# Performance work log

Measured on AMD Instinct MI355X. Metric: run time of the kernel, lower is better.

The kernel has to match this reference:

```python
import jax, jax.numpy as jnp
import numpy as np

NB, FD, NR, L = 4, 128, 4, 4
CUT, CUT3, NE = 5.0, 4.0, 108
N_ATOMS, N_EDGES, N_ANGLES, N_GRAPHS = 8000, 200000, 400000, 100
BONDS_PER, ANGLES_PER = 2000, 4000

def swish(x):
    return x * jax.nn.sigmoid(x)

def cutoff_fn(r, rc):
    x = r / rc
    return 1.0 - 6.0 * x**5 + 15.0 * x**4 - 10.0 * x**3

def rbf(r):
    # smooth Bessel basis, [E, NR+1]
    n = jnp.arange(1, NR + 2, dtype=r.dtype)
    return jnp.sqrt(2.0 / CUT) * jnp.sin(n * jnp.pi * r[:, None] / CUT) / r[:, None]

def shrb(r, cos_t):
    # spherical-harmonic (Legendre, l=0..3) x radial Bessel (n=1..4) -> [A, 16]
    n = jnp.arange(1, NR + 1, dtype=r.dtype)
    rad = jnp.sin(n * jnp.pi * r[:, None] / CUT3) / r[:, None]
    ang = jnp.stack([jnp.ones_like(cos_t), cos_t, 0.5 * (3.0 * cos_t**2 - 1.0), 0.5 * (5.0 * cos_t**3 - 3.0 * cos_t)], axis=1)
    feat = (rad[:, :, None] * ang[:, None, :]).reshape(r.shape[0], NR * L)
    return feat * cutoff_fn(r, CUT3)[:, None]

def setup_inputs() -> dict:
    key = jax.random.key(0)
    ks = jax.random.split(key, 24)
    def nrm(k, shape, fan):
        return jax.random.normal(k, shape, jnp.float32) / np.sqrt(fan).astype(np.float32)
    return {
        'atomic_numbers': jax.random.randint(ks[0], (N_ATOMS,), 0, NE, jnp.int32),
        'edge_index': jax.random.randint(ks[1], (2, N_EDGES), 0, N_ATOMS, jnp.int32),
        'edge_dist': jax.random.uniform(ks[2], (N_EDGES,), jnp.float32, 0.5, CUT),
        'three_body_indices': jax.random.randint(ks[3], (N_ANGLES, 2), 0, BONDS_PER, jnp.int32),
        'norm_ik': jax.random.uniform(ks[4], (N_ANGLES,), jnp.float32, 0.5, CUT3),
        'cos_angles': jax.random.uniform(ks[5], (N_ANGLES,), jnp.float32, -1.0, 1.0),
        'total_num_bonds': jnp.full((N_GRAPHS,), BONDS_PER, jnp.int32),
        'total_num_angles': jnp.full((N_GRAPHS,), ANGLES_PER, jnp.int32),
        'emb': nrm(ks[6], (NE, FD), 1.0),
        'W_enc': nrm(ks[7], (NR + 1, FD), NR + 1), 'b_enc': jnp.zeros((FD,), jnp.float32),
        'W_angle': nrm(ks[8], (NB, NR * L, FD), NR * L),
        'Wg': nrm(ks[9], (NB, FD, FD), FD), 'bg': jnp.zeros((NB, FD), jnp.float32),
        'W_tb': nrm(ks[10], (NB, FD, FD), FD), 'b_tb': jnp.zeros((NB, FD), jnp.float32),
        'We1': nrm(ks[11], (NB, 3 * FD, FD), 3 * FD), 'be1': jnp.zeros((NB, FD), jnp.float32),
        'We0': nrm(ks[12], (NB, NR + 1, FD), NR + 1),
        'Wa1': nrm(ks[13], (NB, 3 * FD, FD), 3 * FD), 'ba1': jnp.zeros((NB, FD), jnp.float32),
        'Wa0': nrm(ks[14], (NB, NR + 1, FD), NR + 1),
        'W1': nrm(ks[15], (FD, FD), FD), 'b1': jnp.zeros((FD,), jnp.float32),
        'W2': nrm(ks[16], (FD, FD), FD), 'b2': jnp.zeros((FD,), jnp.float32),
        'W3': nrm(ks[17], (FD, 1), FD), 'b3': jnp.zeros((1,), jnp.float32),
    }

def reference(atomic_numbers, edge_index, edge_dist, three_body_indices, norm_ik, cos_angles, total_num_bonds, total_num_angles, emb, W_enc, b_enc, W_angle, Wg, bg, W_tb, b_tb, We1, be1, We0, Wa1, ba1, Wa0, W1, b1, W2, b2, W3, b3):
    E, N, A = edge_dist.shape[0], atomic_numbers.shape[0], norm_ik.shape[0]
    # ragged three-body index offsets (cumsum over per-graph bond counts)
    cum = jnp.cumsum(total_num_bonds)
    off = jnp.concatenate([jnp.zeros((1,), cum.dtype), cum[:-1]])
    off_a = jnp.repeat(off, total_num_angles, total_repeat_length=A)
    tbi = three_body_indices + off_a[:, None].astype(three_body_indices.dtype)
    idx_ij, idx_ik = tbi[:, 0], tbi[:, 1]
    send, recv = edge_index[0], edge_index[1]
    ef0 = rbf(edge_dist)                      # [E, 5]
    e = swish(ef0 @ W_enc + b_enc)            # [E, FD]
    v = emb[atomic_numbers]                   # [N, FD]
    ang = shrb(norm_ik, cos_angles)           # [A, 16]
    fc_ik = cutoff_fn(norm_ik, CUT3)          # [A]
    for b in range(NB):
        # three-body interaction: angle -> center bond ij
        k_atom = recv[idx_ik]
        gate = jax.nn.sigmoid(v[k_atom] @ Wg[b] + bg[b])            # [A, FD]
        msg = (ang @ W_angle[b]) * gate * fc_ik[:, None]            # [A, FD]
        agg = jax.ops.segment_sum(msg, idx_ij, num_segments=E)      # [E, FD]
        e = e + swish(agg @ W_tb[b] + b_tb[b])
        # gated graph conv: edge update then atom update
        vi, vj = v[send], v[recv]
        h = jnp.concatenate([vi, vj, e], axis=1)                    # [E, 3FD]
        e = e + swish(h @ We1[b] + be1[b]) * (ef0 @ We0[b])
        h2 = jnp.concatenate([vi, vj, e], axis=1)
        m = swish(h2 @ Wa1[b] + ba1[b]) * (ef0 @ Wa0[b])
        v = v + jax.ops.segment_sum(m, recv, num_segments=N)
    # per-atom energy readout
    h = swish(v @ W1 + b1)
    h = swish(h @ W2 + b2)
    return h @ W3 + b3                                              # [N, 1]
```

## Files before the change

kernel.cpp:

```cpp
#include <hip/hip_runtime.h>


typedef short short8 __attribute__((ext_vector_type(8)));
typedef float f32x4v __attribute__((ext_vector_type(4)));
typedef __bf16 bf16x2_t __attribute__((ext_vector_type(2)));

__device__ __forceinline__ float sigmoidf_(float x) { return 1.0f / (1.0f + __expf(-x)); }
__device__ __forceinline__ float swishf_(float x) { return x * sigmoidf_(x); }

__device__ __forceinline__ unsigned int pk2(float a, float b) {
    bf16x2_t v = {(__bf16)a, (__bf16)b};
    return __builtin_bit_cast(unsigned int, v);
}
__device__ __forceinline__ unsigned short f2bf(float x) {
    return __builtin_bit_cast(unsigned short, (__bf16)x);
}
__device__ __forceinline__ float bf2f(unsigned short u) {
    return __uint_as_float(((unsigned int)u) << 16);
}
__device__ __forceinline__ float blo(unsigned int u) { return __uint_as_float(u << 16); }
__device__ __forceinline__ float bhi(unsigned int u) { return __uint_as_float(u & 0xffff0000u); }
__device__ __forceinline__ unsigned int addbf2(unsigned int a, unsigned int b) {
    return pk2(blo(a) + blo(b), bhi(a) + bhi(b));
}

__device__ __forceinline__ f32x4v mfma_bf16(short8 a, short8 b, f32x4v c) {
    return __builtin_amdgcn_mfma_f32_16x16x32_bf16(a, b, c, 0, 0, 0);
}

__device__ __forceinline__ float4 f4add(float4 a, float4 b) {
    return make_float4(a.x + b.x, a.y + b.y, a.z + b.z, a.w + b.w);
}
__device__ __forceinline__ float4 f4swish(float4 a) {
    return make_float4(swishf_(a.x), swishf_(a.y), swishf_(a.z), swishf_(a.w));
}
__device__ __forceinline__ float getc(const float4& v, int i) {
    return i == 0 ? v.x : (i == 1 ? v.y : (i == 2 ? v.z : v.w));
}

#define FMA4(J, A) \
    acc[J].x = fmaf(A, bv.x, acc[J].x); acc[J].y = fmaf(A, bv.y, acc[J].y); \
    acc[J].z = fmaf(A, bv.z, acc[J].z); acc[J].w = fmaf(A, bv.w, acc[J].w)

template <int S>
__device__ __forceinline__ void gemm32f(const float* As, const float* __restrict__ B,
                                        int tm, int f0, float4 acc[4]) {
#pragma unroll 4
    for (int k = 0; k < 128; ++k) {
        const float4 a0 = *(const float4*)(As + k * S + (tm << 2));
        const float4 bv = *(const float4*)(B + (k << 7) + f0);
        FMA4(0, a0.x); FMA4(1, a0.y); FMA4(2, a0.z); FMA4(3, a0.w);
    }
}

__global__ void k_offsets(const int* __restrict__ tnb, const int* __restrict__ tna,
                          int NG, int* __restrict__ boff, int* __restrict__ acum) {
    if (threadIdx.x == 0 && blockIdx.x == 0) {
        int ab = 0, aa = 0;
        for (int g = 0; g < NG; ++g) {
            boff[g] = ab;
            ab += tnb[g];
            aa += tna[g];
            acum[g] = aa;
        }
    }
}

__global__ void k_hist_ang(const int* __restrict__ tb,
                           const int* __restrict__ boff, const int* __restrict__ acum,
                           int A, int NG, int* __restrict__ cnt) {
    const int a = blockIdx.x * 256 + threadIdx.x;
    if (a >= A) return;
    int lo = 0, hi = NG - 1;
    while (lo < hi) {
        const int mid = (lo + hi) >> 1;
        if (a < acum[mid]) hi = mid; else lo = mid + 1;
    }
    atomicAdd(&cnt[tb[2 * a] + boff[lo]], 1);
}

__global__ void k_angle_scatter(const int* __restrict__ tb, const float* __restrict__ rnorm,
                                const float* __restrict__ cosang, const int* __restrict__ ei,
                                int E, int A, int NG,
                                const int* __restrict__ boff, const int* __restrict__ acum,
                                const int* __restrict__ start, const int* __restrict__ bsumE,
                                int* __restrict__ fill,
                                unsigned short* __restrict__ angS,
                                int* __restrict__ katS) {
    const int a = blockIdx.x * 256 + threadIdx.x;
    if (a >= A) return;
    int lo = 0, hi = NG - 1;
    while (lo < hi) {
        const int mid = (lo + hi) >> 1;
        if (a < acum[mid]) hi = mid; else lo = mid + 1;
    }
    const int off = boff[lo];
    const int ij = tb[2 * a] + off;
    const int kat = ei[(size_t)E + tb[2 * a + 1] + off];
    const int pos = start[ij] + bsumE[ij >> 11] + atomicAdd(&fill[ij], 1);

    const float r = rnorm[a], c = cosang[a];
    const float rinv = 1.0f / r;
    const float x = r * 0.25f;
    const float fc = 1.0f + x * x * x * (-10.0f + x * (15.0f - 6.0f * x));
    const float fc2 = fc * fc;
    const float p2 = 1.5f * c * c - 0.5f;
    const float p3 = 2.5f * c * c * c - 1.5f * c;
    union { unsigned int ui[8]; uint4 v[2]; } pkk;
#pragma unroll
    for (int n = 0; n < 4; ++n) {
        const float rad = __sinf(r * (float)(n + 1) * 0.7853981633974483f) * rinv * fc2;
        pkk.ui[n * 2 + 0] = pk2(rad, rad * c);
        pkk.ui[n * 2 + 1] = pk2(rad * p2, rad * p3);
    }
    uint4* dst = (uint4*)(angS + (size_t)pos * 16);
    dst[0] = pkk.v[0];
    dst[1] = pkk.v[1];
    katS[pos] = kat;
}

__global__ void k_scan1b(const int* __restrict__ cntE, int* __restrict__ startE,
                         int* __restrict__ bsumE, int nE, int nbE,
                         int* __restrict__ fillE,
                         const int* __restrict__ cntRi, int* __restrict__ startRi,
                         int* __restrict__ bsumRi, int nR,
                         int* __restrict__ fillRi) {
    __shared__ int sh[256];
    const int b = blockIdx.x;
    const int* cnt; int* start; int* bsum; int* fill; int n; int blk;
    if (b < nbE) { cnt = cntE;  start = startE;  bsum = bsumE;  fill = fillE;  n = nE; blk = b; }
    else         { cnt = cntRi; start = startRi; bsum = bsumRi; fill = fillRi; n = nR; blk = b - nbE; }
    const int t = threadIdx.x;
    const int base = blk * 2048 + t * 8;
    int v[8], s = 0;
#pragma unroll
    for (int i = 0; i < 8; ++i) { v[i] = (base + i < n) ? cnt[base + i] : 0; s += v[i]; }
    sh[t] = s;
    __syncthreads();
    for (int off = 1; off < 256; off <<= 1) {
        int x = (t >= off) ? sh[t - off] : 0;
        __syncthreads();
        sh[t] += x;
        __syncthreads();
    }
    if (t == 255) bsum[blk] = sh[255];
    int run = sh[t] - s;
#pragma unroll
    for (int i = 0; i < 8; ++i) {
        if (base + i < n) { start[base + i] = run; fill[base + i] = 0; }
        run += v[i];
    }
}

__global__ void k_scan2b(int* __restrict__ bsumE, int nbE,
                         int* __restrict__ bsumRi, int nbR) {
    __shared__ int sh[256];
    int* bsum; int nb;
    if (blockIdx.x == 0) { bsum = bsumE; nb = nbE; }
    else                 { bsum = bsumRi; nb = nbR; }
    const int t = threadIdx.x;
    int v = (t < nb) ? bsum[t] : 0;
    sh[t] = v;
    __syncthreads();
    for (int off = 1; off < 256; off <<= 1) {
        int x = (t >= off) ? sh[t - off] : 0;
        __syncthreads();
        sh[t] += x;
        __syncthreads();
    }
    if (t < nb) bsum[t] = sh[t] - v;
}

__global__ void k_scatter_recv(const int* __restrict__ ei, int E,
                               const int* __restrict__ startR, const int* __restrict__ bsumR,
                               int* __restrict__ fillR,
                               int* __restrict__ epos) {
    const int e = blockIdx.x * 256 + threadIdx.x;
    if (e < E) {
        const int r = ei[(size_t)E + e];
        epos[e] = startR[r] + bsumR[r >> 11] + atomicAdd(&fillR[r], 1);
    }
}

__global__ void k_pack(const float* __restrict__ Wg, const float* __restrict__ Wtb,
                       const float* __restrict__ We1, const float* __restrict__ Wa1,
                       unsigned short* __restrict__ Bpk) {
    const int gid = blockIdx.x * 256 + threadIdx.x;
    const int mat = gid >> 11;
    const int t2 = gid & 2047;
    const int b = mat >> 3, which = mat & 7;
    const float* W;
    switch (which) {
        case 0: W = Wg + (size_t)b * 16384; break;
        case 1: W = We1 + (size_t)b * 49152; break;
        case 2: W = We1 + (size_t)b * 49152 + 16384; break;
        case 3: W = Wa1 + (size_t)b * 49152; break;
        case 4: W = Wa1 + (size_t)b * 49152 + 16384; break;
        case 5: W = Wtb + (size_t)b * 16384; break;
        case 6: W = We1 + (size_t)b * 49152 + 32768; break;
        default: W = Wa1 + (size_t)b * 49152 + 32768; break;
    }
    const int kc = t2 >> 9, nt = (t2 >> 6) & 7, lane = t2 & 63;
    const int q = lane >> 4, cc = lane & 15;
    const int col = nt * 16 + cc;
    union { unsigned short us[8]; uint4 v; } pk;
#pragma unroll
    for (int j = 0; j < 8; ++j)
        pk.us[j] = f2bf(W[(size_t)(kc * 32 + q * 8 + j) * 128 + col]);
    *(uint4*)(Bpk + (size_t)mat * 16384 + (size_t)((kc * 8 + nt) * 64 + lane) * 8) = pk.v;
}

__global__ void k_pack_s(const float* __restrict__ Wang, const float* __restrict__ We0g,
                         const float* __restrict__ Wa0g, unsigned short* __restrict__ Spk) {
    const int gid = blockIdx.x * 64 + threadIdx.x;
    const int m = gid >> 9;
    const int nt = (gid >> 6) & 7, lane = gid & 63;
    const int b = m & 3, type = m >> 2;
    const int q = lane >> 4, cc = lane & 15;
    const int col = nt * 16 + cc;
    const float* W;
    int K;
    if (type == 0)      { W = Wang + (size_t)b * 2048; K = 16; }
    else if (type == 1) { W = We0g + (size_t)b * 640;  K = 5;  }
    else                { W = Wa0g + (size_t)b * 640;  K = 5;  }
    union { unsigned short us[8]; uint4 v; } pk;
#pragma unroll
    for (int j = 0; j < 8; ++j) {
        const int k = q * 8 + j;
        pk.us[j] = (k < K) ? f2bf(W[(size_t)k * 128 + col]) : (unsigned short)0;
    }
    *(uint4*)(Spk + (size_t)m * 4096 + (size_t)(nt * 64 + lane) * 8) = pk.v;
}

__global__ void k_edge_init(const float* __restrict__ dist, const float* __restrict__ Wenc,
                            const float* __restrict__ benc,
                            const int* __restrict__ ei, int E, int* __restrict__ cntR,
                            unsigned int* __restrict__ ePq,
                            unsigned int* __restrict__ ef0q) {
    __shared__ float sarr[16][5];
    const int s = blockIdx.x, t = threadIdx.x;
    if (t < 16) {
        const float r = dist[s * 16 + t];
        const float rinv = 1.0f / r;
        float vv[5];
#pragma unroll
        for (int n = 0; n < 5; ++n) {
            vv[n] = 0.6324555320336759f * __sinf(r * (float)(n + 1) * 0.6283185307179586f) * rinv;
            sarr[t][n] = vv[n];
        }
        uint4 pq;
        pq.x = pk2(vv[0], vv[1]);
        pq.y = pk2(vv[2], vv[3]);
        pq.z = pk2(vv[4], 0.0f);
        pq.w = 0u;
        *(uint4*)(ef0q + (size_t)(s * 16 + t) * 4) = pq;
        atomicAdd(&cntR[ei[(size_t)E + s * 16 + t]], 1);
    }
    __syncthreads();
    const int lane = t >> 3, nt = t & 7;
    const int q = lane >> 4;
    const int f = nt * 16 + (lane & 15);
    float wv[5];
#pragma unroll
    for (int n = 0; n < 5; ++n) wv[n] = Wenc[n * 128 + f];
    const float bz = benc[f];
    float o[4];
#pragma unroll
    for (int r = 0; r < 4; ++r) {
        const int m = q * 4 + r;
        float acc = bz;
#pragma unroll
        for (int n = 0; n < 5; ++n) acc = fmaf(sarr[m][n], wv[n], acc);
        o[r] = swishf_(acc);
    }
    unsigned int* epB = ePq + (size_t)s * 1024;
    epB[(nt * 2) * 64 + lane] = pk2(o[0], o[1]);
    epB[(nt * 2 + 1) * 64 + lane] = pk2(o[2], o[3]);
}

__global__ void k_atom_init(const int* __restrict__ an, const float* __restrict__ emb,
                            float* __restrict__ v, unsigned int* __restrict__ vq, int N) {
    const size_t gid = (size_t)blockIdx.x * 256 + threadIdx.x;
    if (gid >= (size_t)N * 64) return;
    const int a = (int)(gid >> 6), j = (int)(gid & 63);
    const float2 e = *(const float2*)(emb + (size_t)an[a] * 128 + 2 * j);
    *(float2*)(v + (size_t)a * 128 + 2 * j) = e;
    vq[gid] = pk2(e.x, e.y);
}

__global__ void __launch_bounds__(256, 4) k_atom_pre(
    const unsigned int* __restrict__ vq,
    const unsigned short* __restrict__ Bpk5, const float* __restrict__ bg,
    unsigned int* __restrict__ Gq, unsigned int* __restrict__ Pe1q,
    unsigned int* __restrict__ Pe2q,
    unsigned int* __restrict__ Pa1q, unsigned int* __restrict__ Pa2q) {
    __shared__ __align__(16) unsigned short At[64 * 136];
    unsigned int* At32 = (unsigned int*)At;
    const int t = threadIdx.x;
    const int w = t >> 6, l = t & 63;
    const int q = l >> 4, c = l & 15;
    const int g = blockIdx.y;
    const int abase = blockIdx.x * 64 + 16 * w;

    const unsigned short* vh = (const unsigned short*)vq;
    short8 af[4];
#pragma unroll
    for (int kc = 0; kc < 4; ++kc)
        af[kc] = *(const short8*)(vh + (size_t)(abase + c) * 128 + kc * 32 + q * 8);

    const short8* Bp = (const short8*)(Bpk5 + (size_t)g * 16384);
    const f32x4v zz = {0.0f, 0.0f, 0.0f, 0.0f};
    f32x4v acc[8];
#pragma unroll
    for (int nt = 0; nt < 8; ++nt) acc[nt] = zz;
#pragma unroll
    for (int nt = 0; nt < 8; ++nt)
#pragma unroll
        for (int kc = 0; kc < 4; ++kc)
            acc[nt] = mfma_bf16(af[kc], Bp[(kc * 8 + nt) * 64 + l], acc[nt]);

    unsigned int* OUT = (g == 0) ? Gq : (g == 1) ? Pe1q : (g == 2) ? Pe2q
                      : (g == 3) ? Pa1q : Pa2q;
#pragma unroll
    for (int nt = 0; nt < 8; ++nt) {
        const int fo = nt * 16 + c;
        if (g == 0) {
            const float bz = bg[fo];
#pragma unroll
            for (int r = 0; r < 4; ++r)
                At[(16 * w + q * 4 + r) * 136 + fo] = f2bf(sigmoidf_(acc[nt][r] + bz));
        } else {
#pragma unroll
            for (int r = 0; r < 4; ++r)
                At[(16 * w + q * 4 + r) * 136 + fo] = f2bf(acc[nt][r]);
        }
    }
#pragma unroll
    for (int j = 0; j < 16; ++j)
        OUT[(size_t)(abase + j) * 64 + l] = At32[(16 * w + j) * 68 + l];
}

__global__ void __launch_bounds__(128, 4) k_edge(
    const unsigned short* __restrict__ angBS, const int* __restrict__ katS,
    const int* __restrict__ startA, const int* __restrict__ bsumE,
    const int* __restrict__ cntA,
    const unsigned int* __restrict__ Gq, const unsigned short* __restrict__ Wangpk,
    const unsigned int* __restrict__ ef0q,
    unsigned int* __restrict__ ePq, const int* __restrict__ ei, int E,
    const unsigned int* __restrict__ Pe1q, const unsigned int* __restrict__ Pe2q,
    const unsigned int* __restrict__ Pa1q, const unsigned int* __restrict__ Pa2q,
    const int* __restrict__ epos,
    const unsigned short* __restrict__ Bpk3,
    const float* __restrict__ btb, const float* __restrict__ be1,
    const unsigned short* __restrict__ We0pk, const float* __restrict__ ba1,
    const unsigned short* __restrict__ Wa0pk, unsigned int* __restrict__ mPq) {
    __shared__ __align__(16) unsigned short At[32 * 136];
    __shared__ __align__(16) unsigned short sPh[32 * 136];
    __shared__ int sA0[32], sAn[32];
    unsigned int* At32 = (unsigned int*)At;
    unsigned int* sP32 = (unsigned int*)sPh;

    const int t = threadIdx.x;
    const int w = t >> 6, l = t & 63;
    const int q = l >> 4, c = l & 15;
    const int g4 = l >> 4, l16 = l & 15;
    const size_t base = (size_t)blockIdx.x * 32;
    const int wbase = (int)base + 16 * w;
    const f32x4v zz = {0.0f, 0.0f, 0.0f, 0.0f};

    if (l < 16) {
        const int e = wbase + l;
        sA0[16 * w + l] = startA[e] + bsumE[e >> 11];
        sAn[16 * w + l] = cntA[e];
    }

    int eiS[4], eiR[4];
#pragma unroll
    for (int i = 0; i < 4; ++i) {
        eiS[i] = ei[wbase + i * 4 + g4];
        eiR[i] = ei[(size_t)E + wbase + i * 4 + g4];
    }

    short8 afE = {0, 0, 0, 0, 0, 0, 0, 0};
    if (q == 0)
        afE = *(const short8*)((const unsigned short*)ef0q + (size_t)(wbase + c) * 8);

#define STAGE_SP(P1, P2)                                                         \
    _Pragma("unroll") for (int i = 0; i < 4; ++i) {                              \
        const int j = i * 4 + g4;                                                \
        const uint4 u1 = *(const uint4*)((P1) + (size_t)eiS[i] * 64 + l16 * 4);  \
        const uint4 u2 = *(const uint4*)((P2) + (size_t)eiR[i] * 64 + l16 * 4);  \
        uint4 o;                                                                 \
        o.x = addbf2(u1.x, u2.x); o.y = addbf2(u1.y, u2.y);                      \
        o.z = addbf2(u1.z, u2.z); o.w = addbf2(u1.w, u2.w);                      \
        *(uint4*)(sP32 + (16 * w + j) * 68 + l16 * 4) = o;                       \
    }

    unsigned int* epB = ePq + (size_t)(blockIdx.x * 2 + w) * 1024;

    {
        int j = 0;
        const int aBeg = __builtin_amdgcn_readfirstlane(sA0[16 * w]);
        const int aEnd = __builtin_amdgcn_readfirstlane(sA0[16 * w + 15] + sAn[16 * w + 15]);
        int nextB = __builtin_amdgcn_readfirstlane(sA0[16 * w] + sAn[16 * w]);
        float aa0 = 0.0f, aa1 = 0.0f;
        const short8* WB = (const short8*)Wangpk;
        unsigned short* msg = sPh + (16 * w) * 136;
        unsigned int* msg32 = sP32 + (16 * w) * 68;

#define FLUSH_TO(AIDX)                                                           \
        while ((AIDX) >= nextB && j < 15) {                                      \
            At32[(16 * w + j) * 68 + l] = pk2(aa0, aa1);                         \
            aa0 = 0.0f; aa1 = 0.0f;                                              \
            ++j;                                                                 \
            nextB = __builtin_amdgcn_readfirstlane(sA0[16 * w + j] + sAn[16 * w + j]); \
        }

        short8 afN = {0, 0, 0, 0, 0, 0, 0, 0};
        if (aBeg < aEnd && q < 2 && aBeg + c < aEnd)
            afN = *(const short8*)(angBS + (size_t)(aBeg + c) * 16 + q * 8);

        for (int a0 = aBeg; a0 < aEnd; a0 += 16) {
            const short8 afA = afN;
            short8 afZ = {0, 0, 0, 0, 0, 0, 0, 0};
            afN = afZ;
            if (q < 2 && a0 + 16 + c < aEnd)
                afN = *(const short8*)(angBS + (size_t)(a0 + 16 + c) * 16 + q * 8);

            unsigned int gvv[16];
#pragma unroll
            for (int r16 = 0; r16 < 16; ++r16) {
                const int aa = (a0 + r16 < aEnd) ? a0 + r16 : aEnd - 1;
                gvv[r16] = Gq[(size_t)katS[aa] * 64 + l];
            }

#pragma unroll
            for (int nt = 0; nt < 8; ++nt) {
                f32x4v d = mfma_bf16(afA, WB[nt * 64 + l], zz);
#pragma unroll
                for (int r = 0; r < 4; ++r)
                    msg[(q * 4 + r) * 136 + nt * 16 + c] = f2bf(d[r]);
            }
            asm volatile("s_waitcnt lgkmcnt(0)" ::: "memory");
            __builtin_amdgcn_sched_barrier(0);

            unsigned int mvv[16];
#pragma unroll
            for (int r16 = 0; r16 < 16; ++r16) mvv[r16] = msg32[r16 * 68 + l];
            asm volatile("s_waitcnt lgkmcnt(0)" ::: "memory");
            __builtin_amdgcn_sched_barrier(0);

#pragma unroll
            for (int r16 = 0; r16 < 16; ++r16) {
                const int a = a0 + r16;
                FLUSH_TO(a)
                aa0 = fmaf(blo(mvv[r16]), blo(gvv[r16]), aa0);
                aa1 = fmaf(bhi(mvv[r16]), bhi(gvv[r16]), aa1);
            }
        }
        At32[(16 * w + j) * 68 + l] = pk2(aa0, aa1);
        for (int jj = j + 1; jj < 16; ++jj) At32[(16 * w + jj) * 68 + l] = 0u;
#undef FLUSH_TO
    }
    asm volatile("s_waitcnt lgkmcnt(0)" ::: "memory");
    __builtin_amdgcn_sched_barrier(0);

    STAGE_SP(Pe1q, Pe2q)

    const short8* Bp1 = (const short8*)Bpk3;
    const short8* Bp2 = Bp1 + 2048;
    const short8* Bp3 = Bp2 + 2048;
    const short8* W0e = (const short8*)We0pk;
    const short8* W0a = (const short8*)Wa0pk;

    short8 af[4];
#define LOAD_AF                                                                  \
    _Pragma("unroll") for (int kc = 0; kc < 4; ++kc)                             \
        af[kc] = *(const short8*)(At + (16 * w + c) * 136 + kc * 32 + q * 8);
#define TRANSPOSE_ER2                                                            \
    _Pragma("unroll") for (int nt = 0; nt < 8; ++nt) {                           \
        At[(16 * w + q * 4 + 0) * 136 + nt * 16 + c] = (unsigned short)er2[2 * nt];        \
        At[(16 * w + q * 4 + 1) * 136 + nt * 16 + c] = (unsigned short)(er2[2 * nt] >> 16);\
        At[(16 * w + q * 4 + 2) * 136 + nt * 16 + c] = (unsigned short)er2[2 * nt + 1];    \
        At[(16 * w + q * 4 + 3) * 136 + nt * 16 + c] = (unsigned short)(er2[2 * nt + 1] >> 16);\
    }

    unsigned int er2[16];

    LOAD_AF
#pragma unroll 1
    for (int h = 0; h < 2; ++h) {
        unsigned int eold[8];
#pragma unroll
        for (int s = 0; s < 8; ++s) eold[s] = epB[(h * 8 + s) * 64 + l];
        f32x4v acc[4];
#pragma unroll
        for (int n2 = 0; n2 < 4; ++n2) acc[n2] = zz;
#pragma unroll
        for (int n2 = 0; n2 < 4; ++n2)
#pragma unroll
            for (int kc = 0; kc < 4; ++kc)
                acc[n2] = mfma_bf16(af[kc], Bp1[(kc * 8 + h * 4 + n2) * 64 + l], acc[n2]);
#pragma unroll
        for (int n2 = 0; n2 < 4; ++n2) {
            const int nt = h * 4 + n2;
            const unsigned int e0 = eold[2 * n2];
            const unsigned int e1 = eold[2 * n2 + 1];
            const float bt = btb[nt * 16 + c];
            er2[2 * nt] = pk2(blo(e0) + swishf_(acc[n2][0] + bt),
                              bhi(e0) + swishf_(acc[n2][1] + bt));
            er2[2 * nt + 1] = pk2(blo(e1) + swishf_(acc[n2][2] + bt),
                                  bhi(e1) + swishf_(acc[n2][3] + bt));
        }
    }
    TRANSPOSE_ER2

    asm volatile("s_waitcnt lgkmcnt(0)" ::: "memory");
    __builtin_amdgcn_sched_barrier(0);

    LOAD_AF
#pragma unroll 1
    for (int h = 0; h < 2; ++h) {
        f32x4v acc[4];
#pragma unroll
        for (int n2 = 0; n2 < 4; ++n2) acc[n2] = zz;
#pragma unroll
        for (int n2 = 0; n2 < 4; ++n2)
#pragma unroll
            for (int kc = 0; kc < 4; ++kc)
                acc[n2] = mfma_bf16(af[kc], Bp2[(kc * 8 + h * 4 + n2) * 64 + l], acc[n2]);
        f32x4v scv[4];
#pragma unroll
        for (int n2 = 0; n2 < 4; ++n2)
            scv[n2] = mfma_bf16(afE, W0e[(h * 4 + n2) * 64 + l], zz);
#pragma unroll
        for (int n2 = 0; n2 < 4; ++n2) {
            const int nt = h * 4 + n2;
            const int fo = nt * 16 + c;
            const float bt = be1[fo];
            float vv[4];
#pragma unroll
            for (int r = 0; r < 4; ++r) {
                const float p12 = bf2f(sPh[(16 * w + q * 4 + r) * 136 + fo]);
                const float x = acc[n2][r] + bt + p12;
                const unsigned int eold = er2[2 * nt + (r >> 1)];
                const float eb = (r & 1) ? bhi(eold) : blo(eold);
                vv[r] = eb + swishf_(x) * scv[n2][r];
            }
            er2[2 * nt] = pk2(vv[0], vv[1]);
            er2[2 * nt + 1] = pk2(vv[2], vv[3]);
            epB[(2 * nt) * 64 + l] = er2[2 * nt];
            epB[(2 * nt + 1) * 64 + l] = er2[2 * nt + 1];
        }
    }
    STAGE_SP(Pa1q, Pa2q)
    TRANSPOSE_ER2

    LOAD_AF
#pragma unroll 1
    for (int h = 0; h < 2; ++h) {
        f32x4v acc[4];
#pragma unroll
        for (int n2 = 0; n2 < 4; ++n2) acc[n2] = zz;
#pragma unroll
        for (int n2 = 0; n2 < 4; ++n2)
#pragma unroll
            for (int kc = 0; kc < 4; ++kc)
                acc[n2] = mfma_bf16(af[kc], Bp3[(kc * 8 + h * 4 + n2) * 64 + l], acc[n2]);
        f32x4v scv[4];
#pragma unroll
        for (int n2 = 0; n2 < 4; ++n2)
            scv[n2] = mfma_bf16(afE, W0a[(h * 4 + n2) * 64 + l], zz);
#pragma unroll
        for (int n2 = 0; n2 < 4; ++n2) {
            const int nt = h * 4 + n2;
            const int fo = nt * 16 + c;
            const float bt = ba1[fo];
#pragma unroll
            for (int r = 0; r < 4; ++r) {
                const float p12 = bf2f(sPh[(16 * w + q * 4 + r) * 136 + fo]);
                const float x = acc[n2][r] + bt + p12;
                At[(16 * w + q * 4 + r) * 136 + fo] = f2bf(swishf_(x) * scv[n2][r]);
            }
        }
    }
#pragma unroll
    for (int j = 0; j < 16; ++j) {
        const int ep = epos[wbase + j];
        mPq[(size_t)ep * 64 + l] = At32[(16 * w + j) * 68 + l];
    }
#undef LOAD_AF
#undef TRANSPOSE_ER2
#undef STAGE_SP
}

__global__ void k_dvagg(const unsigned int* __restrict__ mPq,
                        const int* __restrict__ startR, const int* __restrict__ bsumR,
                        const int* __restrict__ cntR,
                        float* __restrict__ v, unsigned int* __restrict__ vq, int N) {
    const int a = blockIdx.x * 4 + (threadIdx.x >> 6);
    if (a >= N) return;
    const int l = threadIdx.x & 63;
    const int s0 = startR[a] + bsumR[a >> 11], n = cntR[a];
    float a0 = 0.0f, a1 = 0.0f, b0 = 0.0f, b1 = 0.0f;
    int i = 0;
    for (; i + 4 <= n; i += 4) {
        const unsigned int u0 = mPq[(size_t)(s0 + i + 0) * 64 + l];
        const unsigned int u1 = mPq[(size_t)(s0 + i + 1) * 64 + l];
        const unsigned int u2 = mPq[(size_t)(s0 + i + 2) * 64 + l];
        const unsigned int u3 = mPq[(size_t)(s0 + i + 3) * 64 + l];
        a0 += blo(u0) + blo(u1);
        a1 += bhi(u0) + bhi(u1);
        b0 += blo(u2) + blo(u3);
        b1 += bhi(u2) + bhi(u3);
    }
    for (; i < n; ++i) {
        const unsigned int u = mPq[(size_t)(s0 + i) * 64 + l];
        a0 += blo(u);
        a1 += bhi(u);
    }
    a0 += b0;
    a1 += b1;
    const float v0 = v[(size_t)a * 128 + 2 * l] + a0;
    const float v1 = v[(size_t)a * 128 + 2 * l + 1] + a1;
    v[(size_t)a * 128 + 2 * l] = v0;
    v[(size_t)a * 128 + 2 * l + 1] = v1;
    vq[(size_t)a * 64 + l] = pk2(v0, v1);
}

__global__ void k_readout(const float* __restrict__ v,
                          const float* __restrict__ W1, const float* __restrict__ b1,
                          const float* __restrict__ W2, const float* __restrict__ b2,
                          const float* __restrict__ W3, const float* __restrict__ b3,
                          float* __restrict__ out) {
    __shared__ float At[128 * 36];
    const int t = threadIdx.x;
    const int tn = t & 31, tm = t >> 5;
    const int f0 = tn << 2;
    const size_t base = (size_t)blockIdx.x * 32;
    {
        const int m = t & 31, cb = t >> 5;
        const float4* src = (const float4*)(v + (base + m) * 128);
#pragma unroll
        for (int i = 0; i < 4; ++i) {
            const int c = cb + (i << 3);
            const float4 ld = src[c];
            float* dst = At + (c << 2) * 32 + m;
            dst[0] = ld.x; dst[32] = ld.y; dst[64] = ld.z; dst[96] = ld.w;
        }
    }
    __syncthreads();
    float4 acc[4] = {};
    gemm32f<32>(At, W1, tm, f0, acc);
    {
        const float4 bv1 = *(const float4*)(b1 + f0);
#pragma unroll
        for (int j = 0; j < 4; ++j) acc[j] = f4swish(f4add(acc[j], bv1));
    }
    __syncthreads();
#pragma unroll
    for (int i = 0; i < 4; ++i) {
        float4 w0;
        w0.x = getc(acc[0], i); w0.y = getc(acc[1], i); w0.z = getc(acc[2], i); w0.w = getc(acc[3], i);
        *(float4*)(At + (f0 + i) * 36 + (tm << 2)) = w0;
    }
    __syncthreads();
    float4 acc2[4] = {};
    gemm32f<36>(At, W2, tm, f0, acc2);
    const float4 bv2 = *(const float4*)(b2 + f0);
    const float4 w3v = *(const float4*)(W3 + f0);
#pragma unroll
    for (int j = 0; j < 4; ++j) {
        const float4 h = f4swish(f4add(acc2[j], bv2));
        float p = h.x * w3v.x + h.y * w3v.y + h.z * w3v.z + h.w * w3v.w;
        p += __shfl_xor(p, 16);
        p += __shfl_xor(p, 8);
        p += __shfl_xor(p, 4);
        p += __shfl_xor(p, 2);
        p += __shfl_xor(p, 1);
        if (tn == 0) out[base + (tm << 2) + j] = p + b3[0];
    }
}

extern "C" void kernel_launch(void* const* d_in, const int* in_sizes, int n_in,
                              void* d_out, int out_size, void* d_ws, size_t ws_size,
                              hipStream_t stream) {
    const int N = in_sizes[0];
    const int E = in_sizes[2];
    const int A = in_sizes[4];
    const int NG = in_sizes[6];

    const int* an = (const int*)d_in[0];
    const int* ei = (const int*)d_in[1];
    const float* dist = (const float*)d_in[2];
    const int* tb = (const int*)d_in[3];
    const float* rnorm = (const float*)d_in[4];
    const float* cosang = (const float*)d_in[5];
    const int* tnb = (const int*)d_in[6];
    const int* tna = (const int*)d_in[7];
    const float* emb = (const float*)d_in[8];
    const float* Wenc = (const float*)d_in[9];
    const float* benc = (const float*)d_in[10];
    const float* Wang = (const float*)d_in[11];
    const float* Wg = (const float*)d_in[12];
    const float* bg = (const float*)d_in[13];
    const float* Wtb = (const float*)d_in[14];
    const float* btb = (const float*)d_in[15];
    const float* We1 = (const float*)d_in[16];
    const float* be1 = (const float*)d_in[17];
    const float* We0 = (const float*)d_in[18];
    const float* Wa1 = (const float*)d_in[19];
    const float* ba1 = (const float*)d_in[20];
    const float* Wa0 = (const float*)d_in[21];
    const float* W1 = (const float*)d_in[22];
    const float* b1 = (const float*)d_in[23];
    const float* W2 = (const float*)d_in[24];
    const float* b2 = (const float*)d_in[25];
    const float* W3 = (const float*)d_in[26];
    const float* b3 = (const float*)d_in[27];
    float* out = (float*)d_out;

    float* ws = (float*)d_ws;
    size_t off = 0;
    auto alloc = [&](size_t n) { float* p = ws + off; off += (n + 3) & ~(size_t)3; return p; };
    unsigned int* ePq = (unsigned int*)alloc((size_t)E * 64);
    unsigned int* mPq = (unsigned int*)alloc((size_t)E * 64);
    float* v_ = alloc((size_t)N * 128);
    unsigned int* vq = (unsigned int*)alloc((size_t)N * 64);
    unsigned int* Gq = (unsigned int*)alloc((size_t)N * 64);
    unsigned int* Pe1q = (unsigned int*)alloc((size_t)N * 64);
    unsigned int* Pe2q = (unsigned int*)alloc((size_t)N * 64);
    unsigned int* Pa1q = (unsigned int*)alloc((size_t)N * 64);
    unsigned int* Pa2q = (unsigned int*)alloc((size_t)N * 64);
    unsigned int* ef0q = (unsigned int*)alloc((size_t)E * 4);
    unsigned short* angBS = (unsigned short*)alloc((size_t)A * 8);
    int* katS = (int*)alloc((size_t)A);
    int* cnt = (int*)alloc((size_t)E);
    int* start = (int*)alloc((size_t)E);
    int* fill = (int*)alloc((size_t)E);
    int* cntR = (int*)alloc((size_t)N);
    int* startR = (int*)alloc((size_t)N);
    int* fillR = (int*)alloc((size_t)N);
    int* epos = (int*)alloc((size_t)E);
    int* bsumE = (int*)alloc(512);
    int* bsumR = (int*)alloc(512);
    int* boff = (int*)alloc(256);
    int* acum = boff + 128;
    unsigned short* Bpk = (unsigned short*)alloc((size_t)32 * 8192);
    unsigned short* Spk = (unsigned short*)alloc((size_t)12 * 2048);

    const int nscanE = (E + 2047) / 2048;
    const int nscanR = (N + 2047) / 2048;

    (void)hipMemsetAsync(cnt, 0, (size_t)E * 4, stream);
    (void)hipMemsetAsync(cntR, 0, (size_t)N * 4, stream);
    k_offsets<<<1, 64, 0, stream>>>(tnb, tna, NG, boff, acum);
    k_hist_ang<<<(A + 255) / 256, 256, 0, stream>>>(tb, boff, acum, A, NG, cnt);
    k_edge_init<<<E / 16, 512, 0, stream>>>(dist, Wenc, benc, ei, E, cntR, ePq, ef0q);
    k_scan1b<<<nscanE + nscanR, 256, 0, stream>>>(cnt, start, bsumE, E, nscanE, fill,
                                                  cntR, startR, bsumR, N, fillR);
    k_scan2b<<<2, 256, 0, stream>>>(bsumE, nscanE, bsumR, nscanR);
    k_angle_scatter<<<(A + 255) / 256, 256, 0, stream>>>(tb, rnorm, cosang, ei, E, A, NG,
                                                         boff, acum, start, bsumE, fill,
                                                         angBS, katS);
    k_scatter_recv<<<(E + 255) / 256, 256, 0, stream>>>(ei, E, startR, bsumR, fillR, epos);
    k_pack<<<256, 256, 0, stream>>>(Wg, Wtb, We1, Wa1, Bpk);
    k_pack_s<<<96, 64, 0, stream>>>(Wang, We0, Wa0, Spk);
    k_atom_init<<<(int)(((size_t)N * 64 + 255) / 256), 256, 0, stream>>>(an, emb, v_, vq, N);

    for (int b = 0; b < 4; ++b) {
        k_atom_pre<<<dim3(N / 64, 5), 256, 0, stream>>>(
            vq, Bpk + (size_t)(b * 8) * 16384, bg + b * 128,
            Gq, Pe1q, Pe2q, Pa1q, Pa2q);
        k_edge<<<E / 32, 128, 0, stream>>>(
            angBS, katS, start, bsumE, cnt, Gq, Spk + (size_t)b * 4096, ef0q,
            ePq, ei, E, Pe1q, Pe2q, Pa1q, Pa2q, epos,
            Bpk + (size_t)(b * 8 + 5) * 16384,
            btb + b * 128, be1 + b * 128,
            Spk + (size_t)(4 + b) * 4096, ba1 + b * 128,
            Spk + (size_t)(8 + b) * 4096, mPq);
        k_dvagg<<<(N + 3) / 4, 256, 0, stream>>>(mPq, startR, bsumR, cntR, v_, vq, N);
    }
    k_readout<<<N / 32, 256, 0, stream>>>(v_, W1, b1, W2, b2, W3, b3, out);
}
```

Before: 952.4 us.

## Cache angle edge indices in histogram pass and restructure atom precompute per wave

The histogram kernel now stores each angle's resolved center-bond index and source-bond index, so the scatter kernel no longer repeats the binary search over graphs or re-reads the triplet table. Separately, k_atom_pre becomes a single-wave block of 16 atoms that loops over all five weight groups. The A fragment is loaded once and reused across groups instead of being reloaded per grid-y group. This adds two A-sized int buffers, and the one-wave blocks with serialized group loop may lower occupancy and latency hiding.

```diff
diff --git a/kernel.cpp b/kernel.cpp
--- a/kernel.cpp
+++ b/kernel.cpp
@@ -68,7 +68,8 @@
 
 __global__ void k_hist_ang(const int* __restrict__ tb,
                            const int* __restrict__ boff, const int* __restrict__ acum,
-                           int A, int NG, int* __restrict__ cnt) {
+                           int A, int NG, int* __restrict__ cnt,
+                           int* __restrict__ aij, int* __restrict__ asrc) {
     const int a = blockIdx.x * 256 + threadIdx.x;
     if (a >= A) return;
     int lo = 0, hi = NG - 1;
@@ -76,27 +77,25 @@
         const int mid = (lo + hi) >> 1;
         if (a < acum[mid]) hi = mid; else lo = mid + 1;
     }
-    atomicAdd(&cnt[tb[2 * a] + boff[lo]], 1);
-}
-
-__global__ void k_angle_scatter(const int* __restrict__ tb, const float* __restrict__ rnorm,
+    const int off = boff[lo];
+    const int ij = tb[2 * a] + off;
+    aij[a] = ij;
+    asrc[a] = tb[2 * a + 1] + off;
+    atomicAdd(&cnt[ij], 1);
+}
+
+__global__ void k_angle_scatter(const int* __restrict__ aij, const int* __restrict__ asrc,
+                                const float* __restrict__ rnorm,
                                 const float* __restrict__ cosang, const int* __restrict__ ei,
-                                int E, int A, int NG,
-                                const int* __restrict__ boff, const int* __restrict__ acum,
+                                int E, int A,
                                 const int* __restrict__ start, const int* __restrict__ bsumE,
                                 int* __restrict__ fill,
                                 unsigned short* __restrict__ angS,
                                 int* __restrict__ katS) {
     const int a = blockIdx.x * 256 + threadIdx.x;
     if (a >= A) return;
-    int lo = 0, hi = NG - 1;
-    while (lo < hi) {
-        const int mid = (lo + hi) >> 1;
-        if (a < acum[mid]) hi = mid; else lo = mid + 1;
-    }
-    const int off = boff[lo];
-    const int ij = tb[2 * a] + off;
-    const int kat = ei[(size_t)E + tb[2 * a + 1] + off];
+    const int ij = aij[a];
+    const int kat = ei[(size_t)E + asrc[a]];
     const int pos = start[ij] + bsumE[ij >> 11] + atomicAdd(&fill[ij], 1);
 
     const float r = rnorm[a], c = cosang[a];
@@ -288,19 +287,17 @@
     vq[gid] = pk2(e.x, e.y);
 }
 
-__global__ void __launch_bounds__(256, 4) k_atom_pre(
+__global__ void k_atom_pre(
     const unsigned int* __restrict__ vq,
     const unsigned short* __restrict__ Bpk5, const float* __restrict__ bg,
     unsigned int* __restrict__ Gq, unsigned int* __restrict__ Pe1q,
     unsigned int* __restrict__ Pe2q,
     unsigned int* __restrict__ Pa1q, unsigned int* __restrict__ Pa2q) {
-    __shared__ __align__(16) unsigned short At[64 * 136];
+    __shared__ __align__(16) unsigned short At[16 * 136];
     unsigned int* At32 = (unsigned int*)At;
-    const int t = threadIdx.x;
-    const int w = t >> 6, l = t & 63;
+    const int l = threadIdx.x;
     const int q = l >> 4, c = l & 15;
-    const int g = blockIdx.y;
-    const int abase = blockIdx.x * 64 + 16 * w;
+    const int abase = blockIdx.x * 16;
 
     const unsigned short* vh = (const unsigned short*)vq;
     short8 af[4];
@@ -308,36 +305,43 @@
     for (int kc = 0; kc < 4; ++kc)
         af[kc] = *(const short8*)(vh + (size_t)(abase + c) * 128 + kc * 32 + q * 8);
 
-    const short8* Bp = (const short8*)(Bpk5 + (size_t)g * 16384);
     const f32x4v zz = {0.0f, 0.0f, 0.0f, 0.0f};
-    f32x4v acc[8];
-#pragma unroll
-    for (int nt = 0; nt < 8; ++nt) acc[nt] = zz;
-#pragma unroll
-    for (int nt = 0; nt < 8; ++nt)
-#pragma unroll
-        for (int kc = 0; kc < 4; ++kc)
-            acc[nt] = mfma_bf16(af[kc], Bp[(kc * 8 + nt) * 64 + l], acc[nt]);
-
-    unsigned int* OUT = (g == 0) ? Gq : (g == 1) ? Pe1q : (g == 2) ? Pe2q
-                      : (g == 3) ? Pa1q : Pa2q;
-#pragma unroll
-    for (int nt = 0; nt < 8; ++nt) {
-        const int fo = nt * 16 + c;
-        if (g == 0) {
-            const float bz = bg[fo];
-#pragma unroll
-            for (int r = 0; r < 4; ++r)
-                At[(16 * w + q * 4 + r) * 136 + fo] = f2bf(sigmoidf_(acc[nt][r] + bz));
-        } else {
-#pragma unroll
-            for (int r = 0; r < 4; ++r)
-                At[(16 * w + q * 4 + r) * 136 + fo] = f2bf(acc[nt][r]);
-        }
-    }
-#pragma unroll
-    for (int j = 0; j < 16; ++j)
-        OUT[(size_t)(abase + j) * 64 + l] = At32[(16 * w + j) * 68 + l];
+#pragma unroll
+    for (int g = 0; g < 5; ++g) {
+        const short8* Bp = (const short8*)(Bpk5 + (size_t)g * 16384);
+        f32x4v acc[8];
+#pragma unroll
+        for (int nt = 0; nt < 8; ++nt) acc[nt] = zz;
+#pragma unroll
+        for (int nt = 0; nt < 8; ++nt)
+#pragma unroll
+            for (int kc = 0; kc < 4; ++kc)
+                acc[nt] = mfma_bf16(af[kc], Bp[(kc * 8 + nt) * 64 + l], acc[nt]);
+
+        unsigned int* OUT = (g == 0) ? Gq : (g == 1) ? Pe1q : (g == 2) ? Pe2q
+                          : (g == 3) ? Pa1q : Pa2q;
+#pragma unroll
+        for (int nt = 0; nt < 8; ++nt) {
+            const int fo = nt * 16 + c;
+            if (g == 0) {
+                const float bz = bg[fo];
+#pragma unroll
+                for (int r = 0; r < 4; ++r)
+                    At[(q * 4 + r) * 136 + fo] = f2bf(sigmoidf_(acc[nt][r] + bz));
+            } else {
+#pragma unroll
+                for (int r = 0; r < 4; ++r)
+                    At[(q * 4 + r) * 136 + fo] = f2bf(acc[nt][r]);
+            }
+        }
+        asm volatile("s_waitcnt lgkmcnt(0)" ::: "memory");
+        __builtin_amdgcn_sched_barrier(0);
+#pragma unroll
+        for (int j = 0; j < 16; ++j)
+            OUT[(size_t)(abase + j) * 64 + l] = At32[j * 68 + l];
+        asm volatile("s_waitcnt lgkmcnt(0)" ::: "memory");
+        __builtin_amdgcn_sched_barrier(0);
+    }
 }
 
 __global__ void __launch_bounds__(128, 4) k_edge(
@@ -735,6 +739,8 @@
     unsigned int* ef0q = (unsigned int*)alloc((size_t)E * 4);
     unsigned short* angBS = (unsigned short*)alloc((size_t)A * 8);
     int* katS = (int*)alloc((size_t)A);
+    int* aij = (int*)alloc((size_t)A);
+    int* asrc = (int*)alloc((size_t)A);
     int* cnt = (int*)alloc((size_t)E);
     int* start = (int*)alloc((size_t)E);
     int* fill = (int*)alloc((size_t)E);
@@ -755,21 +761,20 @@
     (void)hipMemsetAsync(cnt, 0, (size_t)E * 4, stream);
     (void)hipMemsetAsync(cntR, 0, (size_t)N * 4, stream);
     k_offsets<<<1, 64, 0, stream>>>(tnb, tna, NG, boff, acum);
-    k_hist_ang<<<(A + 255) / 256, 256, 0, stream>>>(tb, boff, acum, A, NG, cnt);
+    k_hist_ang<<<(A + 255) / 256, 256, 0, stream>>>(tb, boff, acum, A, NG, cnt, aij, asrc);
     k_edge_init<<<E / 16, 512, 0, stream>>>(dist, Wenc, benc, ei, E, cntR, ePq, ef0q);
     k_scan1b<<<nscanE + nscanR, 256, 0, stream>>>(cnt, start, bsumE, E, nscanE, fill,
                                                   cntR, startR, bsumR, N, fillR);
     k_scan2b<<<2, 256, 0, stream>>>(bsumE, nscanE, bsumR, nscanR);
-    k_angle_scatter<<<(A + 255) / 256, 256, 0, stream>>>(tb, rnorm, cosang, ei, E, A, NG,
-                                                         boff, acum, start, bsumE, fill,
-                                                         angBS, katS);
+    k_angle_scatter<<<(A + 255) / 256, 256, 0, stream>>>(aij, asrc, rnorm, cosang, ei, E, A,
+                                                         start, bsumE, fill, angBS, katS);
     k_scatter_recv<<<(E + 255) / 256, 256, 0, stream>>>(ei, E, startR, bsumR, fillR, epos);
     k_pack<<<256, 256, 0, stream>>>(Wg, Wtb, We1, Wa1, Bpk);
     k_pack_s<<<96, 64, 0, stream>>>(Wang, We0, Wa0, Spk);
     k_atom_init<<<(int)(((size_t)N * 64 + 255) / 256), 256, 0, stream>>>(an, emb, v_, vq, N);
 
     for (int b = 0; b < 4; ++b) {
-        k_atom_pre<<<dim3(N / 64, 5), 256, 0, stream>>>(
+        k_atom_pre<<<N / 16, 64, 0, stream>>>(
             vq, Bpk + (size_t)(b * 8) * 16384, bg + b * 128,
             Gq, Pe1q, Pe2q, Pa1q, Pa2q);
         k_edge<<<E / 32, 128, 0, stream>>>(
```

After: 963.6 us. No clear change (+1.2%).
